# Kernel tuning notes

Hardware: AMD Instinct MI355X
Metric: run time of the kernel (lower is better)

Reference implementation:

```python
import jax, jax.numpy as jnp
import numpy as np

C = 1.0                 # Poincare ball curvature
PROJ_EPS = 1e-5         # boundary epsilon for projection
ACOSH_EPS = 1e-7        # numerical floor for arccosh argument


def setup_inputs() -> dict:
    key = jax.random.key(0)
    k1, k2 = jax.random.split(key)
    num_tokens, embed_dim = 30522, 64
    batch, seq = 4, 1024
    token_ids = jax.random.randint(k1, (batch, seq), 0, num_tokens, dtype=jnp.int64)
    weight = jax.random.normal(k2, (num_tokens, embed_dim), dtype=jnp.float32) * 0.05
    scale = jnp.asarray(0.5, dtype=jnp.float32)
    return {"token_ids": token_ids, "weight": weight, "scale": scale}


def _poincare_bias(token_ids, weight, scale):
    ids = jnp.clip(token_ids, 0, weight.shape[0] - 1)
    emb = weight[ids]                                   # (b, s, d)
    # project onto the Poincare ball: clip norm to (1 - eps) / sqrt(c)
    sqc = jnp.sqrt(C)
    max_norm = (1.0 - PROJ_EPS) / sqc
    norm = jnp.linalg.norm(emb, axis=-1, keepdims=True)
    emb = jnp.where(norm > max_norm, emb * (max_norm / jnp.maximum(norm, 1e-12)), emb)
    # pairwise hyperbolic distance via arccosh form (== Mobius-add/artanh form):
    # d(x,y) = (1/sqrt(c)) * arccosh(1 + 2c||x-y||^2 / ((1-c||x||^2)(1-c||y||^2)))
    x2 = jnp.sum(emb * emb, axis=-1)                    # (b, s)
    gram = jnp.einsum("bid,bjd->bij", emb, emb)        # (b, s, s)
    sqdist = jnp.maximum(x2[:, :, None] + x2[:, None, :] - 2.0 * gram, 0.0)
    denom = (1.0 - C * x2)[:, :, None] * (1.0 - C * x2)[:, None, :]
    arg = 1.0 + 2.0 * C * sqdist / denom
    dist = jnp.arccosh(jnp.maximum(arg, 1.0 + ACOSH_EPS)) / sqc
    return scale * -dist                                # (b, s, s)


def reference(token_ids, weight, scale):
    return _poincare_bias(token_ids, weight, scale)
```

## Files before the change

kernel.cpp:

```cpp
#include <hip/hip_runtime.h>
#include <hip/hip_bf16.h>

typedef __attribute__((ext_vector_type(8)))  short bf16x8;
typedef __attribute__((ext_vector_type(4)))  float f32x4;
typedef __attribute__((ext_vector_type(16))) float f32x16;

#define EMB_DIM 64
#define LDS_STRIDE 72

__global__ __launch_bounds__(256) void fused_bias_kernel(
    const int* __restrict__ ids, const float* __restrict__ weight,
    const float* __restrict__ scale_p, float* __restrict__ out,
    int S, int vocab)
{
    __shared__ short Es[128 * LDS_STRIDE];
    __shared__ float x2s[128];

    const int b  = blockIdx.z;
    const int i0 = blockIdx.y * 64;
    const int j0 = blockIdx.x * 64;
    const int t  = threadIdx.x;

    {
        const int r  = t >> 1;
        const int h2 = t & 1;
        const int grow = (r < 64) ? (i0 + r) : (j0 + r - 64);
        int id = ids[(size_t)b * S + grow];
        id = min(max(id, 0), vocab - 1);

        const f32x4* W = (const f32x4*)(weight + (size_t)id * EMB_DIM + h2 * 32);
        f32x4 v[8];
        #pragma unroll
        for (int k = 0; k < 8; ++k) v[k] = W[k];

        float s = 0.f;
        #pragma unroll
        for (int k = 0; k < 8; ++k)
            s += v[k].x * v[k].x + v[k].y * v[k].y + v[k].z * v[k].z + v[k].w * v[k].w;
        s += __shfl_xor(s, 1);

        const float max_norm = 0.99999f;
        float nrm = sqrtf(s);
        float mul = (nrm > max_norm) ? (max_norm / fmaxf(nrm, 1e-12f)) : 1.f;

        const float* vf = (const float*)v;
        bf16x8 hv[4];
        float s2 = 0.f;
        #pragma unroll
        for (int k = 0; k < 32; ++k) {
            __hip_bfloat16 hb = __float2bfloat16(vf[k] * mul);
            float hf = __bfloat162float(hb);
            s2 += hf * hf;
            hv[k >> 3][k & 7] = __builtin_bit_cast(short, hb);
        }
        s2 += __shfl_xor(s2, 1);

        short* dst = Es + r * LDS_STRIDE + h2 * 32;
        #pragma unroll
        for (int k = 0; k < 4; ++k)
            *(bf16x8*)(dst + k * 8) = hv[k];
        if (h2 == 0) x2s[r] = s2;
    }
    __syncthreads();

    const int wid  = t >> 6;
    const int lane = t & 63;
    const int m  = lane & 31;
    const int h  = lane >> 5;
    const int ia = (wid >> 1) * 32;
    const int jb = (wid & 1) * 32;

    const short* Ear = Es + (ia + m) * LDS_STRIDE + h * 8;
    const short* Ebr = Es + (64 + jb + m) * LDS_STRIDE + h * 8;

    f32x16 acc = {};
    #pragma unroll
    for (int kb = 0; kb < 4; ++kb) {
        bf16x8 av = *(const bf16x8*)(Ear + kb * 16);
        bf16x8 bv = *(const bf16x8*)(Ebr + kb * 16);
        acc = __builtin_amdgcn_mfma_f32_32x32x16_bf16(av, bv, acc, 0, 0, 0);
    }

    const float xj    = x2s[64 + jb + m];
    const float scale = scale_p[0];
    const float omxj  = 1.f - xj;

    float* O = out + ((size_t)b * S + i0 + ia + 4 * h) * S + j0 + jb + m;

    #pragma unroll
    for (int g = 0; g < 4; ++g) {
        f32x4 xi4 = *(const f32x4*)(x2s + ia + g * 8 + 4 * h);
        #pragma unroll
        for (int e = 0; e < 4; ++e) {
            float gv = acc[g * 4 + e];
            float xi = xi4[e];
            float sq  = fmaxf(xi + xj - 2.f * gv, 0.f);
            float den = (1.f - xi) * omxj;
            float u = fmaxf(2.f * sq * __builtin_amdgcn_rcpf(den), 1.1920929e-7f);
            float w = 1.f + u + __builtin_amdgcn_sqrtf(u * (u + 2.f));
            float dist = 0.69314718056f * __builtin_amdgcn_logf(w);
            O[(size_t)(g * 8 + e) * S] = -scale * dist;
        }
    }
}

extern "C" void kernel_launch(void* const* d_in, const int* in_sizes, int n_in,
                              void* d_out, int out_size, void* d_ws, size_t ws_size,
                              hipStream_t stream) {
    const int*   ids     = (const int*)d_in[0];
    const float* weight  = (const float*)d_in[1];
    const float* scale_p = (const float*)d_in[2];
    float*       out     = (float*)d_out;

    const int n_tok = in_sizes[0];
    const int vocab = in_sizes[1] / EMB_DIM;
    const int S     = out_size / n_tok;
    const int B     = n_tok / S;

    dim3 grid(S / 64, S / 64, B);
    fused_bias_kernel<<<grid, 256, 0, stream>>>(ids, weight, scale_p, out, S, vocab);
}
```

Baseline: 72.76 us.

## Exploit symmetry: compute upper-triangular tiles and write transposed mirror via LDS

Launches only upper-triangular 64x64 tiles per batch and maps each linear block index to a (ti, tj) tile pair. Each off-diagonal tile writes its result normally and also stages it in LDS transposed, then stores the mirrored tile. This roughly halves the gathers, MFMA work and transcendental math, but every output element is still written. The added LDS round trip, extra barriers and hardcoded 16-tile index math (assumes S=1024) add overhead and reduce generality.

```diff
diff --git a/kernel.cpp b/kernel.cpp
--- a/kernel.cpp
+++ b/kernel.cpp
@@ -2,11 +2,13 @@
 #include <hip/hip_bf16.h>
 
 typedef __attribute__((ext_vector_type(8)))  short bf16x8;
+typedef __attribute__((ext_vector_type(2)))  float f32x2;
 typedef __attribute__((ext_vector_type(4)))  float f32x4;
 typedef __attribute__((ext_vector_type(16))) float f32x16;
 
 #define EMB_DIM 64
 #define LDS_STRIDE 72
+#define LT_STRIDE 66
 
 __global__ __launch_bounds__(256) void fused_bias_kernel(
     const int* __restrict__ ids, const float* __restrict__ weight,
@@ -15,11 +17,21 @@
 {
     __shared__ short Es[128 * LDS_STRIDE];
     __shared__ float x2s[128];
+    float* Lt = (float*)Es;
 
-    const int b  = blockIdx.z;
-    const int i0 = blockIdx.y * 64;
-    const int j0 = blockIdx.x * 64;
-    const int t  = threadIdx.x;
+    const int b = blockIdx.z;
+    {
+    }
+    int tlin = blockIdx.x;
+    int ti = (int)((33.0f - sqrtf(1089.0f - 8.0f * (float)tlin)) * 0.5f);
+    while (16 * (ti + 1) - (ti + 1) * ti / 2 <= tlin) ++ti;
+    while (16 * ti - ti * (ti - 1) / 2 > tlin) --ti;
+    const int tj = ti + (tlin - (16 * ti - ti * (ti - 1) / 2));
+    const int i0 = ti * 64;
+    const int j0 = tj * 64;
+    const bool diag = (ti == tj);
+
+    const int t = threadIdx.x;
 
     {
         const int r  = t >> 1;
@@ -80,6 +92,7 @@
         bf16x8 bv = *(const bf16x8*)(Ebr + kb * 16);
         acc = __builtin_amdgcn_mfma_f32_32x32x16_bf16(av, bv, acc, 0, 0, 0);
     }
+    __syncthreads();
 
     const float xj    = x2s[64 + jb + m];
     const float scale = scale_p[0];
@@ -98,8 +111,25 @@
             float den = (1.f - xi) * omxj;
             float u = fmaxf(2.f * sq * __builtin_amdgcn_rcpf(den), 1.1920929e-7f);
             float w = 1.f + u + __builtin_amdgcn_sqrtf(u * (u + 2.f));
-            float dist = 0.69314718056f * __builtin_amdgcn_logf(w);
-            O[(size_t)(g * 8 + e) * S] = -scale * dist;
+            float val = -scale * (0.69314718056f * __builtin_amdgcn_logf(w));
+            O[(size_t)(g * 8 + e) * S] = val;
+            if (!diag) {
+                int li = ia + 4 * h + g * 8 + e;
+                int lj = jb + m;
+                Lt[lj * LT_STRIDE + li] = val;
+            }
+        }
+    }
+
+    if (!diag) {
+        __syncthreads();
+        const int row0 = t >> 5;
+        const int c2   = (t & 31) * 2;
+        #pragma unroll
+        for (int r8 = 0; r8 < 8; ++r8) {
+            int row = row0 + r8 * 8;
+            f32x2 v2 = *(const f32x2*)(Lt + row * LT_STRIDE + c2);
+            *(f32x2*)(out + ((size_t)b * S + j0 + row) * S + i0 + c2) = v2;
         }
     }
 }
@@ -117,6 +147,7 @@
     const int S     = out_size / n_tok;
     const int B     = n_tok / S;
 
-    dim3 grid(S / 64, S / 64, B);
+    const int NT = S / 64;
+    dim3 grid(NT * (NT + 1) / 2, 1, B);
     fused_bias_kernel<<<grid, 256, 0, stream>>>(ids, weight, scale_p, out, S, vocab);
 }
```

Result: no change. 73.02 us (+0.4%).
